# Performance work log

Measured on AMD Instinct MI355X. Metric: run time of the kernel, lower is better.

## Reference

```python
import jax, jax.numpy as jnp
import numpy as np

B, T = 256, 1024
IN, OUT = 1, 1
H0, H1 = 256, 256


def _lstm_cell(x_t, h, c, W_ih, W_hh, b_ih, b_hh):
    # gates: [B, 4H] in torch LSTMCell order i, f, g, o
    g = x_t @ W_ih.T + b_ih + h @ W_hh.T + b_hh
    i, f, gg, o = jnp.split(g, 4, axis=-1)
    c_new = jax.nn.sigmoid(f) * c + jax.nn.sigmoid(i) * jnp.tanh(gg)
    h_new = jax.nn.sigmoid(o) * jnp.tanh(c_new)
    return h_new, c_new


def setup_inputs() -> dict:
    key = jax.random.key(0)
    ks = jax.random.split(key, 12)
    s = 0.1
    return {
        "x": jax.random.normal(ks[0], (B, T), dtype=jnp.float32),
        "W_ih0": jax.random.normal(ks[1], (4 * H0, IN), dtype=jnp.float32) * s,
        "W_hh0": jax.random.normal(ks[2], (4 * H0, H0), dtype=jnp.float32) * s,
        "b_ih0": jax.random.normal(ks[3], (4 * H0,), dtype=jnp.float32) * s,
        "b_hh0": jax.random.normal(ks[4], (4 * H0,), dtype=jnp.float32) * s,
        "W_ih1": jax.random.normal(ks[5], (4 * H1, H0), dtype=jnp.float32) * s,
        "W_hh1": jax.random.normal(ks[6], (4 * H1, H1), dtype=jnp.float32) * s,
        "b_ih1": jax.random.normal(ks[7], (4 * H1,), dtype=jnp.float32) * s,
        "b_hh1": jax.random.normal(ks[8], (4 * H1,), dtype=jnp.float32) * s,
        "W_lin": jax.random.normal(ks[9], (OUT, H1), dtype=jnp.float32) * s,
        "b_lin": jax.random.normal(ks[10], (OUT,), dtype=jnp.float32) * s,
        "future": 0,
    }


def reference(x, W_ih0, W_hh0, b_ih0, b_hh0, W_ih1, W_hh1, b_ih1, b_hh1,
              W_lin, b_lin, future):
    b = x.shape[0]
    h0 = jnp.zeros((b, H0), x.dtype)
    c0 = jnp.zeros((b, H0), x.dtype)
    h1 = jnp.zeros((b, H1), x.dtype)
    c1 = jnp.zeros((b, H1), x.dtype)

    def step(carry, x_t):
        ht, ct, gt, bt = carry
        ht, ct = _lstm_cell(x_t, ht, ct, W_ih0, W_hh0, b_ih0, b_hh0)
        gt, bt = _lstm_cell(ht, gt, bt, W_ih1, W_hh1, b_ih1, b_hh1)
        out = gt @ W_lin.T + b_lin  # [B, OUT]
        return (ht, ct, gt, bt), out

    xs = x.T[:, :, None]  # [T, B, 1]
    carry, outs = jax.lax.scan(step, (h0, c0, h1, c1), xs)

    if future > 0:
        def fstep(carry, _):
            state, out = carry
            state, out = step(state, out)
            return (state, out), out
        (_, _), fouts = jax.lax.scan(fstep, (carry, outs[-1]), None, length=future)
        outs = jnp.concatenate([outs, fouts], axis=0)

    # stack dim 1 then squeeze(2): [B, T+future]
    return jnp.transpose(outs, (1, 0, 2)).squeeze(2)
```

## Files before the change

### kernel.cpp

```cpp
#include <hip/hip_runtime.h>
#include <hip/hip_bf16.h>
#include <stdint.h>


#define TT   1024
#define NC   16
#define MR   16

typedef __attribute__((ext_vector_type(8))) short  bfrag;
typedef __attribute__((ext_vector_type(4))) float  ffrag;

__device__ __forceinline__ float sigf(float v){ return 1.f/(1.f+__expf(-v)); }
__device__ __forceinline__ float tanhfast(float v){
    v = fminf(fmaxf(v,-15.f),15.f);
    float e = __expf(2.f*v);
    return (e-1.f)/(e+1.f);
}
__device__ __forceinline__ void st32(uint32_t* p, uint32_t v){
    __hip_atomic_store(p, v, __ATOMIC_RELAXED, __HIP_MEMORY_SCOPE_AGENT);
}
__device__ __forceinline__ void st64(unsigned long long* p, unsigned long long v){
    __hip_atomic_store(p, v, __ATOMIC_RELAXED, __HIP_MEMORY_SCOPE_AGENT);
}
__device__ __forceinline__ void stf(float* p, float v){
    __hip_atomic_store(p, v, __ATOMIC_RELAXED, __HIP_MEMORY_SCOPE_AGENT);
}
__device__ __forceinline__ float ldf_coh(const float* p){
    float v;
    __asm__ volatile("global_load_dword %0, %1, off sc0 sc1\n\ts_waitcnt vmcnt(0)"
                     : "=v"(v) : "v"(p) : "memory");
    return v;
}
__device__ __forceinline__ void drain_vmem(){
    __asm__ volatile("s_waitcnt vmcnt(0)" ::: "memory");
}

__device__ __forceinline__ void wave_poll(const int* fa, const int* fb,
                                          const int* fc, const int* fd,
                                          int tgtA, int tgtB){
    for (;;) {
        int a, b, c, d;
        __asm__ volatile(
            "global_load_dword %0, %4, off sc0 sc1\n\t"
            "global_load_dword %1, %5, off sc0 sc1\n\t"
            "global_load_dword %2, %6, off sc0 sc1\n\t"
            "global_load_dword %3, %7, off sc0 sc1\n\t"
            "s_waitcnt vmcnt(0)"
            : "=&v"(a), "=&v"(b), "=&v"(c), "=&v"(d)
            : "v"(fa), "v"(fb), "v"(fc), "v"(fd) : "memory");
        if (a >= tgtA && b >= tgtA && c >= tgtB && d >= tgtB) break;
        __builtin_amdgcn_s_sleep(1);
    }
}

__device__ __forceinline__ void stage_tile(uint32_t* ldsbase, const uint32_t* hblocks,
                                           int kt, int lane){
    const uint32_t* g = hblocks + (kt << 8) + ((lane & 15) << 4) + ((lane >> 4) << 2);
    uint32_t* l = ldsbase + (kt << 8);
    __builtin_amdgcn_global_load_lds(
        (const __attribute__((address_space(1))) uint32_t*)(uintptr_t)g,
        (__attribute__((address_space(3))) uint32_t*)(uint32_t)(uintptr_t)l,
        16, 0, 0x11);
}

__global__ void __launch_bounds__(256, 1)
lstm_kernel(const float* __restrict__ x,
            const float* __restrict__ Wih0, const float* __restrict__ Whh0,
            const float* __restrict__ bih0, const float* __restrict__ bhh0,
            const float* __restrict__ Wih1, const float* __restrict__ Whh1,
            const float* __restrict__ bih1, const float* __restrict__ bhh1,
            const float* __restrict__ Wlin, const float* __restrict__ blin,
            float* __restrict__ out, char* __restrict__ ws)
{
    const int tid = threadIdx.x;
    const int wg  = blockIdx.x;
    const int c   = wg >> 4;
    const int j   = wg & 15;
    const bool isL0 = (j < 8);
    const int  u0   = (isL0 ? j : (j - 8)) * 32;

    int* flagbase = (int*)(ws + c * 4096);
    uint32_t* h0w = (uint32_t*)(ws + 65536);
    uint32_t* h1w = h0w + 4 * NC * 8 * 256;
    float*    op  = (float*)(h1w + 4 * NC * 8 * 256);

    __shared__ __attribute__((aligned(16))) char S[157056];
    __hip_bfloat16* Wt   = (__hip_bfloat16*)S;
    __hip_bfloat16* Wt2  = (__hip_bfloat16*)(S + 65536);
    float*          xs   = (float*)(S + 65536);
    uint32_t*       hs0  = (uint32_t*)(S + 131072);
    uint32_t*       hs1  = (uint32_t*)(S + 139264);
    float*          gbuf = (float*)(S + 147456);
    float*          biasS= (float*)(S + 155904);
    float*          wxS  = (float*)(S + 156416);
    float*          sblin= (float*)(S + 156928);

    {
        const float* Wsrc = isL0 ? Whh0 : Wih1;
        for (int i = tid; i < 128 * 256; i += 256) {
            int n = i >> 8, k = i & 255;
            int r = (n >> 5) * 256 + u0 + (n & 31);
            int lane = (n & 15) | (((k >> 3) & 3) << 4);
            int toff = ((n >> 4) * 8 + (k >> 5)) * 1024 + lane * 16 + (k & 7) * 2;
            *(__hip_bfloat16*)((char*)Wt + toff) = __float2bfloat16(Wsrc[r * 256 + k]);
            if (!isL0)
                *(__hip_bfloat16*)((char*)Wt2 + toff) = __float2bfloat16(Whh1[r * 256 + k]);
        }
        if (isL0) {
            for (int i = tid; i < 16 * 1024; i += 256)
                xs[i] = x[(c * 16 + (i >> 10)) * TT + (i & 1023)];
        }
        if (tid < 128) {
            int r = (tid >> 5) * 256 + u0 + (tid & 31);
            if (isL0) { biasS[tid] = bih0[r] + bhh0[r]; wxS[tid] = Wih0[r]; }
            else      { biasS[tid] = bih1[r] + bhh1[r]; if (tid < 32) wxS[tid] = Wlin[u0 + tid]; }
        }
        if (tid == 0) sblin[0] = blin[0];
        {
            uint32_t* z = isL0 ? (h0w + ((3 * NC + c) * 8 + j) * 256)
                               : (h1w + ((3 * NC + c) * 8 + (j - 8)) * 256);
            st32(z + tid, 0u);
        }
        drain_vmem();
        __syncthreads();
        if (tid == 0) st32((uint32_t*)(flagbase + j * 32), 0u);
    }

    const int lane = tid & 63, wave = tid >> 6;
    const int nt0 = wave * 2, nt1 = wave * 2 + 1;
    const int drow = (lane >> 4) * 4, dcol = lane & 15;
    const int em = tid >> 4, up = tid & 15;
    const int* fL0a = flagbase + (wave)      * 32;
    const int* fL0b = flagbase + (wave + 4)  * 32;
    const int* fL1a = flagbase + (8 + wave)  * 32;
    const int* fL1b = flagbase + (12 + wave) * 32;

    float c0a = 0.f, c0b = 0.f;

    for (int t = 0; t < TT; ++t) {
        if (isL0) {
            wave_poll(fL0a, fL0b, fL1a, fL1b, t, t - 2);
            const uint32_t* src = h0w + (((t + 3) & 3) * NC + c) * 8 * 256;
            stage_tile(hs0, src, wave, lane);
            stage_tile(hs0, src, wave + 4, lane);
            __syncthreads();

            if (t >= 3 && j == ((t - 3) & 7) && tid < 128) {
                int m = tid >> 3, jj = tid & 7;
                float v = ldf_coh(&op[(((t - 3) & 3) * NC + c) * 128 + jj * 16 + m]);
                v += __shfl_down(v, 4, 8);
                v += __shfl_down(v, 2, 8);
                v += __shfl_down(v, 1, 8);
                if (jj == 0) out[(c * 16 + m) * TT + (t - 3)] = v + sblin[0];
            }

            ffrag a0 = {0.f,0.f,0.f,0.f}, a1 = {0.f,0.f,0.f,0.f};
            #pragma unroll
            for (int kt = 0; kt < 8; ++kt) {
                bfrag av = *(const bfrag*)((const char*)hs0 + kt * 1024 + lane * 16);
                bfrag b0 = *(const bfrag*)((const char*)Wt + (nt0 * 8 + kt) * 1024 + lane * 16);
                bfrag b1 = *(const bfrag*)((const char*)Wt + (nt1 * 8 + kt) * 1024 + lane * 16);
                a0 = __builtin_amdgcn_mfma_f32_16x16x32_bf16(av, b0, a0, 0, 0, 0);
                a1 = __builtin_amdgcn_mfma_f32_16x16x32_bf16(av, b1, a1, 0, 0, 0);
            }
            #pragma unroll
            for (int i = 0; i < 4; ++i) {
                gbuf[(drow + i) * 132 + nt0 * 16 + dcol] = a0[i];
                gbuf[(drow + i) * 132 + nt1 * 16 + dcol] = a1[i];
            }
            __syncthreads();

            float2 g_i = *(float2*)(gbuf + em * 132 +      2 * up);
            float2 g_f = *(float2*)(gbuf + em * 132 + 32 + 2 * up);
            float2 g_g = *(float2*)(gbuf + em * 132 + 64 + 2 * up);
            float2 g_o = *(float2*)(gbuf + em * 132 + 96 + 2 * up);
            float xv = xs[em * 1024 + t];
            float i0 = g_i.x + xv * wxS[     2*up  ] + biasS[     2*up  ];
            float i1 = g_i.y + xv * wxS[     2*up+1] + biasS[     2*up+1];
            float f0 = g_f.x + xv * wxS[32 + 2*up  ] + biasS[32 + 2*up  ];
            float f1 = g_f.y + xv * wxS[32 + 2*up+1] + biasS[32 + 2*up+1];
            float gg0 = g_g.x + xv * wxS[64 + 2*up  ] + biasS[64 + 2*up  ];
            float gg1 = g_g.y + xv * wxS[64 + 2*up+1] + biasS[64 + 2*up+1];
            float o0 = g_o.x + xv * wxS[96 + 2*up  ] + biasS[96 + 2*up  ];
            float o1 = g_o.y + xv * wxS[96 + 2*up+1] + biasS[96 + 2*up+1];
            c0a = sigf(f0) * c0a + sigf(i0) * tanhfast(gg0);
            c0b = sigf(f1) * c0b + sigf(i1) * tanhfast(gg1);
            float hn0 = sigf(o0) * tanhfast(c0a);
            float hn1 = sigf(o1) * tanhfast(c0b);
            __hip_bfloat16 hb0 = __float2bfloat16(hn0), hb1 = __float2bfloat16(hn1);
            uint32_t pk = ((uint32_t)(*(uint16_t*)&hb1) << 16) | (uint32_t)(*(uint16_t*)&hb0);
            uint32_t nb = __shfl_down(pk, 1);
            if ((up & 1) == 0) {
                unsigned long long v = (unsigned long long)pk |
                                       ((unsigned long long)nb << 32);
                st64((unsigned long long*)
                     (h0w + (((t & 3) * NC + c) * 8 + j) * 256 + em * 16 + up), v);
            }
            drain_vmem();
            __syncthreads();
            if (tid == 0) st32((uint32_t*)(flagbase + j * 32), (uint32_t)(t + 1));
        } else {
            wave_poll(fL0a, fL0b, fL1a, fL1b, t + 1, t);
            const uint32_t* s0 = h0w + ((t & 3) * NC + c) * 8 * 256;
            const uint32_t* s1 = h1w + (((t + 3) & 3) * NC + c) * 8 * 256;
            stage_tile(hs0, s0, wave, lane);
            stage_tile(hs0, s0, wave + 4, lane);
            stage_tile(hs1, s1, wave, lane);
            stage_tile(hs1, s1, wave + 4, lane);
            __syncthreads();

            ffrag a0 = {0.f,0.f,0.f,0.f}, a1 = {0.f,0.f,0.f,0.f};
            #pragma unroll
            for (int kt = 0; kt < 8; ++kt) {
                bfrag av = *(const bfrag*)((const char*)hs0 + kt * 1024 + lane * 16);
                bfrag b0 = *(const bfrag*)((const char*)Wt + (nt0 * 8 + kt) * 1024 + lane * 16);
                bfrag b1 = *(const bfrag*)((const char*)Wt + (nt1 * 8 + kt) * 1024 + lane * 16);
                a0 = __builtin_amdgcn_mfma_f32_16x16x32_bf16(av, b0, a0, 0, 0, 0);
                a1 = __builtin_amdgcn_mfma_f32_16x16x32_bf16(av, b1, a1, 0, 0, 0);
            }
            #pragma unroll
            for (int kt = 0; kt < 8; ++kt) {
                bfrag av = *(const bfrag*)((const char*)hs1 + kt * 1024 + lane * 16);
                bfrag b0 = *(const bfrag*)((const char*)Wt2 + (nt0 * 8 + kt) * 1024 + lane * 16);
                bfrag b1 = *(const bfrag*)((const char*)Wt2 + (nt1 * 8 + kt) * 1024 + lane * 16);
                a0 = __builtin_amdgcn_mfma_f32_16x16x32_bf16(av, b0, a0, 0, 0, 0);
                a1 = __builtin_amdgcn_mfma_f32_16x16x32_bf16(av, b1, a1, 0, 0, 0);
            }
            #pragma unroll
            for (int i = 0; i < 4; ++i) {
                gbuf[(drow + i) * 132 + nt0 * 16 + dcol] = a0[i];
                gbuf[(drow + i) * 132 + nt1 * 16 + dcol] = a1[i];
            }
            __syncthreads();

            float2 g_i = *(float2*)(gbuf + em * 132 +      2 * up);
            float2 g_f = *(float2*)(gbuf + em * 132 + 32 + 2 * up);
            float2 g_g = *(float2*)(gbuf + em * 132 + 64 + 2 * up);
            float2 g_o = *(float2*)(gbuf + em * 132 + 96 + 2 * up);
            float i0 = g_i.x + biasS[     2*up  ], i1 = g_i.y + biasS[     2*up+1];
            float f0 = g_f.x + biasS[32 + 2*up  ], f1 = g_f.y + biasS[32 + 2*up+1];
            float gg0 = g_g.x + biasS[64 + 2*up ], gg1 = g_g.y + biasS[64 + 2*up+1];
            float o0 = g_o.x + biasS[96 + 2*up  ], o1 = g_o.y + biasS[96 + 2*up+1];
            c0a = sigf(f0) * c0a + sigf(i0) * tanhfast(gg0);
            c0b = sigf(f1) * c0b + sigf(i1) * tanhfast(gg1);
            float hn0 = sigf(o0) * tanhfast(c0a);
            float hn1 = sigf(o1) * tanhfast(c0b);
            __hip_bfloat16 hb0 = __float2bfloat16(hn0), hb1 = __float2bfloat16(hn1);
            uint32_t pk = ((uint32_t)(*(uint16_t*)&hb1) << 16) | (uint32_t)(*(uint16_t*)&hb0);
            uint32_t nb = __shfl_down(pk, 1);
            if ((up & 1) == 0) {
                unsigned long long v = (unsigned long long)pk |
                                       ((unsigned long long)nb << 32);
                st64((unsigned long long*)
                     (h1w + (((t & 3) * NC + c) * 8 + (j - 8)) * 256 + em * 16 + up), v);
            }
            float pv = hn0 * wxS[2 * up] + hn1 * wxS[2 * up + 1];
            pv += __shfl_down(pv, 8, 16);
            pv += __shfl_down(pv, 4, 16);
            pv += __shfl_down(pv, 2, 16);
            pv += __shfl_down(pv, 1, 16);
            if (up == 0)
                stf(&op[((t & 3) * NC + c) * 128 + (j - 8) * 16 + em], pv);
            drain_vmem();
            __syncthreads();
            if (tid == 0) st32((uint32_t*)(flagbase + j * 32), (uint32_t)(t + 1));
        }
    }

    if (isL0 && j >= 5) {
        wave_poll(fL0a, fL0b, fL1a, fL1b, 0, TT);
        __syncthreads();
        int col = TT - 8 + j;
        if (tid < 128) {
            int m = tid >> 3, jj = tid & 7;
            float v = ldf_coh(&op[((col & 3) * NC + c) * 128 + jj * 16 + m]);
            v += __shfl_down(v, 4, 8);
            v += __shfl_down(v, 2, 8);
            v += __shfl_down(v, 1, 8);
            if (jj == 0) out[(c * 16 + m) * TT + col] = v + sblin[0];
        }
    }
}

extern "C" void kernel_launch(void* const* d_in, const int* in_sizes, int n_in,
                              void* d_out, int out_size, void* d_ws, size_t ws_size,
                              hipStream_t stream)
{
    const float* x    = (const float*)d_in[0];
    const float* Wih0 = (const float*)d_in[1];
    const float* Whh0 = (const float*)d_in[2];
    const float* bih0 = (const float*)d_in[3];
    const float* bhh0 = (const float*)d_in[4];
    const float* Wih1 = (const float*)d_in[5];
    const float* Whh1 = (const float*)d_in[6];
    const float* bih1 = (const float*)d_in[7];
    const float* bhh1 = (const float*)d_in[8];
    const float* Wlin = (const float*)d_in[9];
    const float* blin = (const float*)d_in[10];
    float* out = (float*)d_out;
    char* ws   = (char*)d_ws;

    lstm_kernel<<<dim3(256), dim3(256), 0, stream>>>(
        x, Wih0, Whh0, bih0, bhh0, Wih1, Whh1, bih1, bhh1, Wlin, blin, out, ws);
}
```

Before: 3.225 ms.

## Use per-wave flags with vectorized polling and split layer-1 waits

Replaces the block-wide barrier before each flag publish with per-wave flags, each wave writing its own slot once its stores drain. Pollers read four flags per line with dwordx4 loads, and the s_sleep backoff is removed. Layer-1 blocks now wait for and stage their own recurrent h1 tile before waiting on the layer-0 h0 tile. Layer 0 moves its output reduction after the flag publish so it leaves the critical path. This trims barrier and handoff latency on the serial time loop, in exchange for more polling traffic from tight spinning.

```diff
diff --git a/kernel.cpp b/kernel.cpp
--- a/kernel.cpp
+++ b/kernel.cpp
@@ -9,6 +9,7 @@
 
 typedef __attribute__((ext_vector_type(8))) short  bfrag;
 typedef __attribute__((ext_vector_type(4))) float  ffrag;
+typedef __attribute__((ext_vector_type(4))) int    ifrag;
 
 __device__ __forceinline__ float sigf(float v){ return 1.f/(1.f+__expf(-v)); }
 __device__ __forceinline__ float tanhfast(float v){
@@ -35,21 +36,36 @@
     __asm__ volatile("s_waitcnt vmcnt(0)" ::: "memory");
 }
 
-__device__ __forceinline__ void wave_poll(const int* fa, const int* fb,
-                                          const int* fc, const int* fd,
-                                          int tgtA, int tgtB){
+__device__ __forceinline__ void wave_poll4(const int* fa, const int* fb,
+                                           const int* fc, const int* fd,
+                                           int tgtA, int tgtB){
     for (;;) {
-        int a, b, c, d;
+        ifrag A, B, C, D;
         __asm__ volatile(
-            "global_load_dword %0, %4, off sc0 sc1\n\t"
-            "global_load_dword %1, %5, off sc0 sc1\n\t"
-            "global_load_dword %2, %6, off sc0 sc1\n\t"
-            "global_load_dword %3, %7, off sc0 sc1\n\t"
+            "global_load_dwordx4 %0, %4, off sc0 sc1\n\t"
+            "global_load_dwordx4 %1, %5, off sc0 sc1\n\t"
+            "global_load_dwordx4 %2, %6, off sc0 sc1\n\t"
+            "global_load_dwordx4 %3, %7, off sc0 sc1\n\t"
             "s_waitcnt vmcnt(0)"
-            : "=&v"(a), "=&v"(b), "=&v"(c), "=&v"(d)
+            : "=&v"(A), "=&v"(B), "=&v"(C), "=&v"(D)
             : "v"(fa), "v"(fb), "v"(fc), "v"(fd) : "memory");
-        if (a >= tgtA && b >= tgtA && c >= tgtB && d >= tgtB) break;
-        __builtin_amdgcn_s_sleep(1);
+        if (A[0] >= tgtA && A[1] >= tgtA && A[2] >= tgtA && A[3] >= tgtA &&
+            B[0] >= tgtA && B[1] >= tgtA && B[2] >= tgtA && B[3] >= tgtA &&
+            C[0] >= tgtB && C[1] >= tgtB && C[2] >= tgtB && C[3] >= tgtB &&
+            D[0] >= tgtB && D[1] >= tgtB && D[2] >= tgtB && D[3] >= tgtB) break;
+    }
+}
+__device__ __forceinline__ void wave_poll2(const int* fa, const int* fb, int tgt){
+    for (;;) {
+        ifrag A, B;
+        __asm__ volatile(
+            "global_load_dwordx4 %0, %2, off sc0 sc1\n\t"
+            "global_load_dwordx4 %1, %3, off sc0 sc1\n\t"
+            "s_waitcnt vmcnt(0)"
+            : "=&v"(A), "=&v"(B)
+            : "v"(fa), "v"(fb) : "memory");
+        if (A[0] >= tgt && A[1] >= tgt && A[2] >= tgt && A[3] >= tgt &&
+            B[0] >= tgt && B[1] >= tgt && B[2] >= tgt && B[3] >= tgt) break;
     }
 }
 
@@ -95,13 +111,23 @@
     float*          wxS  = (float*)(S + 156416);
     float*          sblin= (float*)(S + 156928);
 
+    const int lane = tid & 63, wave = tid >> 6;
+    const int nt0 = wave * 2, nt1 = wave * 2 + 1;
+    const int drow = (lane >> 4) * 4, dcol = lane & 15;
+    const int em = tid >> 4, up = tid & 15;
+    uint32_t* myflagline = (uint32_t*)(flagbase + j * 32);
+    const int* fL0a = flagbase + (wave)      * 32;
+    const int* fL0b = flagbase + (wave + 4)  * 32;
+    const int* fL1a = flagbase + (8 + wave)  * 32;
+    const int* fL1b = flagbase + (12 + wave) * 32;
+
     {
         const float* Wsrc = isL0 ? Whh0 : Wih1;
         for (int i = tid; i < 128 * 256; i += 256) {
             int n = i >> 8, k = i & 255;
             int r = (n >> 5) * 256 + u0 + (n & 31);
-            int lane = (n & 15) | (((k >> 3) & 3) << 4);
-            int toff = ((n >> 4) * 8 + (k >> 5)) * 1024 + lane * 16 + (k & 7) * 2;
+            int ln = (n & 15) | (((k >> 3) & 3) << 4);
+            int toff = ((n >> 4) * 8 + (k >> 5)) * 1024 + ln * 16 + (k & 7) * 2;
             *(__hip_bfloat16*)((char*)Wt + toff) = __float2bfloat16(Wsrc[r * 256 + k]);
             if (!isL0)
                 *(__hip_bfloat16*)((char*)Wt2 + toff) = __float2bfloat16(Whh1[r * 256 + k]);
@@ -122,37 +148,18 @@
             st32(z + tid, 0u);
         }
         drain_vmem();
-        __syncthreads();
-        if (tid == 0) st32((uint32_t*)(flagbase + j * 32), 0u);
-    }
-
-    const int lane = tid & 63, wave = tid >> 6;
-    const int nt0 = wave * 2, nt1 = wave * 2 + 1;
-    const int drow = (lane >> 4) * 4, dcol = lane & 15;
-    const int em = tid >> 4, up = tid & 15;
-    const int* fL0a = flagbase + (wave)      * 32;
-    const int* fL0b = flagbase + (wave + 4)  * 32;
-    const int* fL1a = flagbase + (8 + wave)  * 32;
-    const int* fL1b = flagbase + (12 + wave) * 32;
+        if (lane == 0) st32(myflagline + wave, 0u);
+    }
 
     float c0a = 0.f, c0b = 0.f;
 
     for (int t = 0; t < TT; ++t) {
         if (isL0) {
-            wave_poll(fL0a, fL0b, fL1a, fL1b, t, t - 2);
+            wave_poll4(fL0a, fL0b, fL1a, fL1b, t, t - 2);
             const uint32_t* src = h0w + (((t + 3) & 3) * NC + c) * 8 * 256;
             stage_tile(hs0, src, wave, lane);
             stage_tile(hs0, src, wave + 4, lane);
             __syncthreads();
-
-            if (t >= 3 && j == ((t - 3) & 7) && tid < 128) {
-                int m = tid >> 3, jj = tid & 7;
-                float v = ldf_coh(&op[(((t - 3) & 3) * NC + c) * 128 + jj * 16 + m]);
-                v += __shfl_down(v, 4, 8);
-                v += __shfl_down(v, 2, 8);
-                v += __shfl_down(v, 1, 8);
-                if (jj == 0) out[(c * 16 + m) * TT + (t - 3)] = v + sblin[0];
-            }
 
             ffrag a0 = {0.f,0.f,0.f,0.f}, a1 = {0.f,0.f,0.f,0.f};
             #pragma unroll
@@ -197,16 +204,25 @@
                      (h0w + (((t & 3) * NC + c) * 8 + j) * 256 + em * 16 + up), v);
             }
             drain_vmem();
-            __syncthreads();
-            if (tid == 0) st32((uint32_t*)(flagbase + j * 32), (uint32_t)(t + 1));
+            if (lane == 0) st32(myflagline + wave, (uint32_t)(t + 1));
+
+            if (t >= 3 && j == ((t - 3) & 7) && tid < 128) {
+                int m = tid >> 3, jj = tid & 7;
+                float v = ldf_coh(&op[(((t - 3) & 3) * NC + c) * 128 + jj * 16 + m]);
+                v += __shfl_down(v, 4, 8);
+                v += __shfl_down(v, 2, 8);
+                v += __shfl_down(v, 1, 8);
+                if (jj == 0) out[(c * 16 + m) * TT + (t - 3)] = v + sblin[0];
+            }
         } else {
-            wave_poll(fL0a, fL0b, fL1a, fL1b, t + 1, t);
+            wave_poll2(fL1a, fL1b, t);
+            const uint32_t* s1 = h1w + (((t + 3) & 3) * NC + c) * 8 * 256;
+            stage_tile(hs1, s1, wave, lane);
+            stage_tile(hs1, s1, wave + 4, lane);
+            wave_poll2(fL0a, fL0b, t + 1);
             const uint32_t* s0 = h0w + ((t & 3) * NC + c) * 8 * 256;
-            const uint32_t* s1 = h1w + (((t + 3) & 3) * NC + c) * 8 * 256;
             stage_tile(hs0, s0, wave, lane);
             stage_tile(hs0, s0, wave + 4, lane);
-            stage_tile(hs1, s1, wave, lane);
-            stage_tile(hs1, s1, wave + 4, lane);
             __syncthreads();
 
             ffrag a0 = {0.f,0.f,0.f,0.f}, a1 = {0.f,0.f,0.f,0.f};
@@ -262,13 +278,12 @@
             if (up == 0)
                 stf(&op[((t & 3) * NC + c) * 128 + (j - 8) * 16 + em], pv);
             drain_vmem();
-            __syncthreads();
-            if (tid == 0) st32((uint32_t*)(flagbase + j * 32), (uint32_t)(t + 1));
+            if (lane == 0) st32(myflagline + wave, (uint32_t)(t + 1));
         }
     }
 
     if (isL0 && j >= 5) {
-        wave_poll(fL0a, fL0b, fL1a, fL1b, 0, TT);
+        wave_poll2(fL1a, fL1b, TT);
         __syncthreads();
         int col = TT - 8 + j;
         if (tid < 128) {
```

After: 3.580 ms. 1.11x slower.
